# Kernel tuning notes

Hardware: AMD Instinct MI355X
Metric: run time of the kernel (lower is better)

The kernel has to match this reference:

```python
import jax, jax.numpy as jnp
import numpy as np

B, S, D = 4, 2048, 1024
H = 16
HD = D // H  # 64
FF = 4096


def setup_inputs() -> dict:
    key = jax.random.key(0)
    ks = jax.random.split(key, 11)
    sd = 1.0 / np.sqrt(D)
    inp = {
        "embeddings": jax.random.normal(ks[0], (B, S, D), dtype=jnp.float32),
        # per-head Linear weights stacked: [H, head_dim, D] (torch Linear layout)
        "Wq": jax.random.uniform(ks[1], (H, HD, D), jnp.float32, -sd, sd),
        "bq": jax.random.uniform(ks[2], (H, HD), jnp.float32, -sd, sd),
        "Wk": jax.random.uniform(ks[3], (H, HD, D), jnp.float32, -sd, sd),
        "bk": jax.random.uniform(ks[4], (H, HD), jnp.float32, -sd, sd),
        "Wv": jax.random.uniform(ks[5], (H, HD, D), jnp.float32, -sd, sd),
        "bv": jax.random.uniform(ks[6], (H, HD), jnp.float32, -sd, sd),
        "W1": jax.random.uniform(ks[7], (FF, D), jnp.float32, -sd, sd),
        "b1": jax.random.uniform(ks[8], (FF,), jnp.float32, -sd, sd),
        "W2": jax.random.uniform(ks[9], (D, FF), jnp.float32, -1.0 / np.sqrt(FF), 1.0 / np.sqrt(FF)),
        "b2": jax.random.uniform(ks[10], (D,), jnp.float32, -1.0 / np.sqrt(FF), 1.0 / np.sqrt(FF)),
    }
    return inp


def reference(embeddings, Wq, bq, Wk, bk, Wv, bv, W1, b1, W2, b2):
    # Per-head projections, batched over heads: [B,H,S,HD]
    Q = jnp.einsum("bsd,hed->bhse", embeddings, Wq) + bq[None, :, None, :]
    K = jnp.einsum("bsd,hed->bhse", embeddings, Wk) + bk[None, :, None, :]
    V = jnp.einsum("bsd,hed->bhse", embeddings, Wv) + bv[None, :, None, :]
    # NOTE: original scales by sqrt(embed_dim), not sqrt(head_dim)
    scale = 1.0 / jnp.sqrt(jnp.asarray(D, embeddings.dtype))
    scores = jnp.einsum("bhse,bhte->bhst", Q, K) * scale  # [B,H,S,S]
    A = jax.nn.softmax(scores, axis=-1)
    Hh = jnp.einsum("bhst,bhte->bhse", A, V)  # [B,H,S,HD]
    # concat heads along last dim (head order matches torch.cat)
    Hcat = jnp.transpose(Hh, (0, 2, 1, 3)).reshape(B, S, D)
    hid = jax.nn.relu(Hcat @ W1.T + b1)
    return hid @ W2.T + b2
```

## Files before the change

### kernel.cpp

```cpp
#include <hip/hip_runtime.h>
#include <stdint.h>


typedef __attribute__((ext_vector_type(8))) short bf16x8;
typedef __attribute__((ext_vector_type(4))) float f32x4;

__device__ __forceinline__ float bf2f(unsigned short u) {
  union { float f; uint32_t i; } v; v.i = ((uint32_t)u) << 16; return v.f;
}
__device__ __forceinline__ unsigned short f2bf(float f) {
  union { float f; uint32_t i; } v; v.f = f;
  uint32_t i = v.i;
  return (unsigned short)((i + 0x7fffu + ((i >> 16) & 1u)) >> 16);
}

#if __has_builtin(__builtin_amdgcn_exp2f)
#define EXP2(x) __builtin_amdgcn_exp2f(x)
#else
#define EXP2(x) __expf((x) * 0.6931471805599453f)
#endif

__device__ __forceinline__ uint32_t pk_bf16(float p0, float p1) {
  union { float f; uint32_t i; } a, b; a.f = p0; b.f = p1;
  return __builtin_amdgcn_perm(b.i + 0x8000u, a.i + 0x8000u, 0x07060302u);
}

__device__ __forceinline__ void gld16(const void* g, void* l) {
  __builtin_amdgcn_global_load_lds(
      (const __attribute__((address_space(1))) uint32_t*)(uintptr_t)g,
      (__attribute__((address_space(3))) uint32_t*)(uintptr_t)l, 16, 0, 0);
}

#define SCALE_Q 0.04508422002778011f

#define W1B          0
#define W2B    4194304
#define B1B    8388608
#define B2B    8392704
#define BQB    8393728
#define BKB    8394752
#define BVB    8395776
#define EMBB   8396800
#define WQB   16785408
#define WKB   17833984
#define WVB   18882560
#define QOFF  19931136
#define KOFF  28319744
#define VTOFF 36708352
#define HCOFF 45096960
#define HIDOFF 8396800

__global__ void cvt_all(const float* __restrict__ emb, const float* __restrict__ Wq,
                        const float* __restrict__ bq,  const float* __restrict__ Wk,
                        const float* __restrict__ bk,  const float* __restrict__ Wv,
                        const float* __restrict__ bv,  const float* __restrict__ W1,
                        const float* __restrict__ b1,  const float* __restrict__ W2,
                        const float* __restrict__ b2,  unsigned short* __restrict__ ws) {
  const int i4 = blockIdx.x * 256 + threadIdx.x;
  if (i4 >= 4982784) return;
  const float* s; unsigned short* d; int base;
  if      (i4 < 2097152) { s = emb; d = ws + EMBB; base = 0; }
  else if (i4 < 2359296) { s = Wq;  d = ws + WQB;  base = 2097152; }
  else if (i4 < 2621440) { s = Wk;  d = ws + WKB;  base = 2359296; }
  else if (i4 < 2883584) { s = Wv;  d = ws + WVB;  base = 2621440; }
  else if (i4 < 3932160) { s = W1;  d = ws + W1B;  base = 2883584; }
  else if (i4 < 4980736) { s = W2;  d = ws + W2B;  base = 3932160; }
  else if (i4 < 4980992) { s = bq;  d = ws + BQB;  base = 4980736; }
  else if (i4 < 4981248) { s = bk;  d = ws + BKB;  base = 4980992; }
  else if (i4 < 4981504) { s = bv;  d = ws + BVB;  base = 4981248; }
  else if (i4 < 4982528) { s = b1;  d = ws + B1B;  base = 4981504; }
  else                   { s = b2;  d = ws + B2B;  base = 4982528; }
  const int j = i4 - base;
  const float4 v = ((const float4*)s)[j];
  ushort4 o;
  o.x = f2bf(v.x); o.y = f2bf(v.y); o.z = f2bf(v.z); o.w = f2bf(v.w);
  *(ushort4*)(d + (size_t)j * 4) = o;
}

template <int MODE>
__launch_bounds__(256, 4)
__global__ void gemm128(const unsigned short* __restrict__ A,
                        const unsigned short* __restrict__ W0,
                        const unsigned short* __restrict__ W1p,
                        const unsigned short* __restrict__ W2p,
                        const unsigned short* __restrict__ bias0,
                        const unsigned short* __restrict__ bias1,
                        const unsigned short* __restrict__ bias2,
                        unsigned short* __restrict__ out0,
                        unsigned short* __restrict__ out1,
                        unsigned short* __restrict__ out2,
                        float* __restrict__ foutp,
                        int N, int K) {
  __shared__ unsigned short At[128 * 64];
  __shared__ unsigned short Bt[128 * 64];
  const int tid  = threadIdx.x;
  const int wave = tid >> 6, lane = tid & 63;
  const int quad = lane >> 4, l15 = lane & 15;

  const int lid = blockIdx.x + blockIdx.y * gridDim.x;
  const int s_ = lid >> 3;
  const int rowBase = (((lid & 7) + ((s_ & 7) << 3)) << 7);
  const int colBase = ((s_ >> 3) << 7);

  const unsigned short* W = W0;
  const unsigned short* bias = bias0;
  int colW = colBase;
  if (MODE == 2) {
    const int which = colBase >> 10;
    if (which == 1) { W = W1p; bias = bias1; }
    if (which == 2) { W = W2p; bias = bias2; }
    colW = colBase & 1023;
  }

  const unsigned short* gA[4]; const unsigned short* gB[4];
  unsigned short *lA[4], *lB[4];
#pragma unroll
  for (int i = 0; i < 4; ++i) {
    const int u = tid + 256 * i;
    const int r = u >> 3, e = (((u & 7) ^ (r & 7)) * 8);
    gA[i] = A + (size_t)(rowBase + r) * K + e;
    gB[i] = W + (size_t)(colW + r) * K + e;
    lA[i] = At + u * 8;
    lB[i] = Bt + u * 8;
  }

  const int wrow = (wave & 1) * 64, wcol = (wave >> 1) * 64;
  int aoff[2][4], boff[2][4];
#pragma unroll
  for (int kk = 0; kk < 2; ++kk)
#pragma unroll
    for (int t = 0; t < 4; ++t) {
      const int ra = wrow + t * 16 + l15;
      aoff[kk][t] = ra * 64 + (((quad + 4 * kk) ^ (ra & 7)) * 8);
      const int rb = wcol + t * 16 + l15;
      boff[kk][t] = rb * 64 + (((quad + 4 * kk) ^ (rb & 7)) * 8);
    }

  f32x4 acc[4][4] = {};
  for (int k0 = 0; k0 < K; k0 += 64) {
    __syncthreads();
#pragma unroll
    for (int i = 0; i < 4; ++i) { gld16(gA[i], lA[i]); gld16(gB[i], lB[i]); }
#pragma unroll
    for (int i = 0; i < 4; ++i) { gA[i] += 64; gB[i] += 64; }
    __syncthreads();
#pragma unroll
    for (int kk = 0; kk < 2; ++kk) {
      bf16x8 af[4], bfr[4];
#pragma unroll
      for (int t = 0; t < 4; ++t) af[t]  = *(const bf16x8*)(At + aoff[kk][t]);
#pragma unroll
      for (int t = 0; t < 4; ++t) bfr[t] = *(const bf16x8*)(Bt + boff[kk][t]);
#pragma unroll
      for (int mt = 0; mt < 4; ++mt)
#pragma unroll
        for (int nt = 0; nt < 4; ++nt)
          acc[mt][nt] = __builtin_amdgcn_mfma_f32_16x16x32_bf16(
              af[mt], bfr[nt], acc[mt][nt], 0, 0, 0);
    }
  }

#pragma unroll
  for (int mt = 0; mt < 4; ++mt) {
    const int row = rowBase + wrow + mt * 16 + quad * 4;
#pragma unroll
    for (int nt = 0; nt < 4; ++nt) {
      const int cIn = colW + wcol + nt * 16 + l15;
      const float bv = bf2f(bias[cIn]);
      if (MODE == 2) {
        const int which = colBase >> 10;
        const int h = cIn >> 6, e = cIn & 63;
#pragma unroll
        for (int r = 0; r < 4; ++r) {
          const int tok = row + r;
          const int b = tok >> 11, s = tok & 2047;
          const float v = acc[mt][nt][r] + bv;
          const size_t bh = (size_t)(b * 16 + h);
          if (which == 0)      out0[(bh * 2048 + s) * 64 + e] = f2bf(v * SCALE_Q);
          else if (which == 1) out1[(bh * 2048 + s) * 64 + e] = f2bf(v);
          else                 out2[(bh * 64 + e) * 2048 + s] = f2bf(v);
        }
      } else if (MODE == 1) {
#pragma unroll
        for (int r = 0; r < 4; ++r) {
          const float v = fmaxf(acc[mt][nt][r] + bv, 0.0f);
          out0[(size_t)(row + r) * N + cIn] = f2bf(v);
        }
      } else {
#pragma unroll
        for (int r = 0; r < 4; ++r)
          foutp[(size_t)(row + r) * N + cIn] = acc[mt][nt][r] + bv;
      }
    }
  }
}

__launch_bounds__(256, 4)
__global__ void flash_attn(const unsigned short* __restrict__ Q,
                           const unsigned short* __restrict__ Kg,
                           const unsigned short* __restrict__ Vt,
                           unsigned short* __restrict__ Hc) {
  __shared__ unsigned short Kt[64 * 64];
  __shared__ unsigned short Vs[64 * 64];
  __shared__ unsigned short Pl[4][32 * 64];
  __shared__ float Lb[4][32];
  const int tid  = threadIdx.x;
  const int wave = tid >> 6, lane = tid & 63;
  const int quad = lane >> 4, l15 = lane & 15;

  const int lid = blockIdx.x + blockIdx.y * gridDim.x;
  const int s_ = lid >> 3;
  const int bh = (lid & 7) + ((s_ & 7) << 3);
  const int q0 = ((s_ >> 3) << 7) + wave * 32;

  const size_t base = (size_t)bh * (2048 * 64);
  const unsigned short* Qb = Q  + base;
  const unsigned short* Kb = Kg + base;
  const unsigned short* Vb = Vt + base;

  bf16x8 qf[2][2];
#pragma unroll
  for (int qt = 0; qt < 2; ++qt) {
    const int q = q0 + qt * 16 + l15;
#pragma unroll
    for (int kk = 0; kk < 2; ++kk)
      qf[qt][kk] = *(const bf16x8*)(Qb + (size_t)q * 64 + kk * 32 + quad * 8);
  }

  const int u0 = tid, u1 = tid + 256;
  const int kr0 = u0 >> 3, kc0 = (((u0 & 7) ^ (kr0 & 7)) * 8);
  const int kr1 = u1 >> 3, kc1 = (((u1 & 7) ^ (kr1 & 7)) * 8);
  const unsigned short* gK0 = Kb + (size_t)kr0 * 64 + kc0;
  const unsigned short* gK1 = Kb + (size_t)kr1 * 64 + kc1;
  const unsigned short* gV0 = Vb + (size_t)kr0 * 2048 + kc0;
  const unsigned short* gV1 = Vb + (size_t)kr1 * 2048 + kc1;
  unsigned short* lK0 = Kt + u0 * 8;
  unsigned short* lK1 = Kt + u1 * 8;
  unsigned short* lV0 = Vs + u0 * 8;
  unsigned short* lV1 = Vs + u1 * 8;

  float l_acc[2] = {0.0f, 0.0f};
  f32x4 o[2][4] = {};
  unsigned short* Pw = Pl[wave];

  for (int it = 0; it < 32; ++it) {
    __syncthreads();
    gld16(gK0, lK0); gld16(gK1, lK1);
    gld16(gV0, lV0); gld16(gV1, lV1);
    gK0 += 4096; gK1 += 4096; gV0 += 64; gV1 += 64;
    __syncthreads();

    f32x4 st[4][2] = {};
#pragma unroll
    for (int tt = 0; tt < 4; ++tt) {
      const int t = tt * 16 + l15;
      const bf16x8 kf0 = *(const bf16x8*)(Kt + t * 64 + ((quad       ^ (t & 7)) * 8));
      const bf16x8 kf1 = *(const bf16x8*)(Kt + t * 64 + (((quad + 4) ^ (t & 7)) * 8));
#pragma unroll
      for (int qt = 0; qt < 2; ++qt) {
        st[tt][qt] = __builtin_amdgcn_mfma_f32_16x16x32_bf16(kf0, qf[qt][0], st[tt][qt], 0, 0, 0);
        st[tt][qt] = __builtin_amdgcn_mfma_f32_16x16x32_bf16(kf1, qf[qt][1], st[tt][qt], 0, 0, 0);
      }
    }

#pragma unroll
    for (int tt = 0; tt < 4; ++tt) {
      const int tc = tt * 2 + (quad >> 1);
#pragma unroll
      for (int qt = 0; qt < 2; ++qt) {
        const float p0 = EXP2(st[tt][qt][0]);
        const float p1 = EXP2(st[tt][qt][1]);
        const float p2 = EXP2(st[tt][qt][2]);
        const float p3 = EXP2(st[tt][qt][3]);
        l_acc[qt] += (p0 + p1) + (p2 + p3);
        uint2 w;
        w.x = pk_bf16(p0, p1);
        w.y = pk_bf16(p2, p3);
        const int qrow = qt * 16 + l15;
        *(uint2*)(Pw + qrow * 64 + ((tc ^ (qrow & 7)) * 8) + (quad & 1) * 4) = w;
      }
    }

    bf16x8 pf[2][2];
#pragma unroll
    for (int mt = 0; mt < 2; ++mt) {
      const int qq = mt * 16 + l15;
      pf[mt][0] = *(const bf16x8*)(Pw + qq * 64 + ((quad       ^ (qq & 7)) * 8));
      pf[mt][1] = *(const bf16x8*)(Pw + qq * 64 + (((quad + 4) ^ (qq & 7)) * 8));
    }
#pragma unroll
    for (int nt = 0; nt < 4; ++nt) {
      const int e = nt * 16 + l15;
      const bf16x8 vf0 = *(const bf16x8*)(Vs + e * 64 + ((quad       ^ (e & 7)) * 8));
      const bf16x8 vf1 = *(const bf16x8*)(Vs + e * 64 + (((quad + 4) ^ (e & 7)) * 8));
#pragma unroll
      for (int mt = 0; mt < 2; ++mt) {
        o[mt][nt] = __builtin_amdgcn_mfma_f32_16x16x32_bf16(pf[mt][0], vf0, o[mt][nt], 0, 0, 0);
        o[mt][nt] = __builtin_amdgcn_mfma_f32_16x16x32_bf16(pf[mt][1], vf1, o[mt][nt], 0, 0, 0);
      }
    }
  }

#pragma unroll
  for (int qt = 0; qt < 2; ++qt) {
    float v = l_acc[qt];
    v += __shfl_xor(v, 16, 64);
    v += __shfl_xor(v, 32, 64);
    Lb[wave][qt * 16 + l15] = v;
  }
  const f32x4 lv0 = *(const f32x4*)&Lb[wave][quad * 4];
  const f32x4 lv1 = *(const f32x4*)&Lb[wave][16 + quad * 4];

  const int b = bh >> 4, h = bh & 15;
#pragma unroll
  for (int mt = 0; mt < 2; ++mt)
#pragma unroll
    for (int r = 0; r < 4; ++r) {
      const int qg = q0 + mt * 16 + quad * 4 + r;
      const float inv = __builtin_amdgcn_rcpf(mt == 0 ? lv0[r] : lv1[r]);
#pragma unroll
      for (int nt = 0; nt < 4; ++nt) {
        const int e = nt * 16 + l15;
        Hc[((size_t)b * 2048 + qg) * 1024 + h * 64 + e] = f2bf(o[mt][nt][r] * inv);
      }
    }
}

extern "C" void kernel_launch(void* const* d_in, const int* in_sizes, int n_in,
                              void* d_out, int out_size, void* d_ws, size_t ws_size,
                              hipStream_t stream) {
  const float* emb = (const float*)d_in[0];
  const float* Wq  = (const float*)d_in[1];
  const float* bq  = (const float*)d_in[2];
  const float* Wk  = (const float*)d_in[3];
  const float* bk  = (const float*)d_in[4];
  const float* Wv  = (const float*)d_in[5];
  const float* bv  = (const float*)d_in[6];
  const float* W1  = (const float*)d_in[7];
  const float* b1  = (const float*)d_in[8];
  const float* W2  = (const float*)d_in[9];
  const float* b2  = (const float*)d_in[10];

  unsigned short* ws = (unsigned short*)d_ws;
  float* out = (float*)d_out;

  cvt_all<<<19465, 256, 0, stream>>>(emb, Wq, bq, Wk, bk, Wv, bv, W1, b1, W2, b2, ws);
  gemm128<2><<<dim3(24, 64), 256, 0, stream>>>(
      ws + EMBB, ws + WQB, ws + WKB, ws + WVB, ws + BQB, ws + BKB, ws + BVB,
      ws + QOFF, ws + KOFF, ws + VTOFF, nullptr, 3072, 1024);
  flash_attn<<<dim3(16, 64), 256, 0, stream>>>(ws + QOFF, ws + KOFF, ws + VTOFF, ws + HCOFF);
  gemm128<1><<<dim3(32, 64), 256, 0, stream>>>(
      ws + HCOFF, ws + W1B, nullptr, nullptr, ws + B1B, nullptr, nullptr,
      ws + HIDOFF, nullptr, nullptr, nullptr, 4096, 1024);
  gemm128<0><<<dim3(8, 64), 256, 0, stream>>>(
      ws + HIDOFF, ws + W2B, nullptr, nullptr, ws + B2B, nullptr, nullptr,
      nullptr, nullptr, nullptr, out, 1024, 4096);
}
```

Baseline: 405.6 us.

## Double-buffer K tiles, overlap V loads, compute row sums via MFMA

The attention kernel now double-buffers K in shared memory, prefetching the next K tile during the current QK^T compute. V is loaded after the PV step, and explicit vmcnt waits with raw barriers replace the two full syncthreads per iteration. The softmax row sum is now computed by an MFMA against a vector of ones, which removes the scalar accumulation and the shuffle/LDS reduction. It also uses the hardware bf16 pack instruction and raises wave priority around MFMA blocks. The trade-offs are more shared memory and hand-written wait counts that must match the issued loads exactly, plus a row sum taken from bf16-rounded probabilities.

```diff
diff --git a/kernel.cpp b/kernel.cpp
--- a/kernel.cpp
+++ b/kernel.cpp
@@ -20,9 +20,10 @@
 #define EXP2(x) __expf((x) * 0.6931471805599453f)
 #endif
 
-__device__ __forceinline__ uint32_t pk_bf16(float p0, float p1) {
-  union { float f; uint32_t i; } a, b; a.f = p0; b.f = p1;
-  return __builtin_amdgcn_perm(b.i + 0x8000u, a.i + 0x8000u, 0x07060302u);
+__device__ __forceinline__ uint32_t cvtpk(float p0, float p1) {
+  uint32_t r;
+  asm("v_cvt_pk_bf16_f32 %0, %1, %2" : "=v"(r) : "v"(p0), "v"(p1));
+  return r;
 }
 
 __device__ __forceinline__ void gld16(const void* g, void* l) {
@@ -200,10 +201,9 @@
                            const unsigned short* __restrict__ Kg,
                            const unsigned short* __restrict__ Vt,
                            unsigned short* __restrict__ Hc) {
-  __shared__ unsigned short Kt[64 * 64];
+  __shared__ unsigned short Kt[2 * 64 * 64];
   __shared__ unsigned short Vs[64 * 64];
   __shared__ unsigned short Pl[4][32 * 64];
-  __shared__ float Lb[4][32];
   const int tid  = threadIdx.x;
   const int wave = tid >> 6, lane = tid & 63;
   const int quad = lane >> 4, l15 = lane & 15;
@@ -239,29 +239,38 @@
   unsigned short* lV0 = Vs + u0 * 8;
   unsigned short* lV1 = Vs + u1 * 8;
 
-  float l_acc[2] = {0.0f, 0.0f};
+  gld16(gK0, lK0); gld16(gK1, lK1);
+  gld16(gV0, lV0); gld16(gV1, lV1);
+  gK0 += 4096; gK1 += 4096; gV0 += 64; gV1 += 64;
+  __syncthreads();
+
+  const short oneb = (short)0x3F80;
+  const bf16x8 ones = {oneb, oneb, oneb, oneb, oneb, oneb, oneb, oneb};
   f32x4 o[2][4] = {};
+  f32x4 lacc[2] = {};
   unsigned short* Pw = Pl[wave];
 
   for (int it = 0; it < 32; ++it) {
-    __syncthreads();
-    gld16(gK0, lK0); gld16(gK1, lK1);
-    gld16(gV0, lV0); gld16(gV1, lV1);
-    gK0 += 4096; gK1 += 4096; gV0 += 64; gV1 += 64;
-    __syncthreads();
+    const int nb = ((it + 1) & 1) * 4096;
+    gld16(gK0, lK0 + nb); gld16(gK1, lK1 + nb);
+    gK0 += 4096; gK1 += 4096;
+
+    const unsigned short* Kc = Kt + (it & 1) * 4096;
 
     f32x4 st[4][2] = {};
+    __builtin_amdgcn_s_setprio(1);
 #pragma unroll
     for (int tt = 0; tt < 4; ++tt) {
       const int t = tt * 16 + l15;
-      const bf16x8 kf0 = *(const bf16x8*)(Kt + t * 64 + ((quad       ^ (t & 7)) * 8));
-      const bf16x8 kf1 = *(const bf16x8*)(Kt + t * 64 + (((quad + 4) ^ (t & 7)) * 8));
+      const bf16x8 kf0 = *(const bf16x8*)(Kc + t * 64 + ((quad       ^ (t & 7)) * 8));
+      const bf16x8 kf1 = *(const bf16x8*)(Kc + t * 64 + (((quad + 4) ^ (t & 7)) * 8));
 #pragma unroll
       for (int qt = 0; qt < 2; ++qt) {
         st[tt][qt] = __builtin_amdgcn_mfma_f32_16x16x32_bf16(kf0, qf[qt][0], st[tt][qt], 0, 0, 0);
         st[tt][qt] = __builtin_amdgcn_mfma_f32_16x16x32_bf16(kf1, qf[qt][1], st[tt][qt], 0, 0, 0);
       }
     }
+    __builtin_amdgcn_s_setprio(0);
 
 #pragma unroll
     for (int tt = 0; tt < 4; ++tt) {
@@ -272,14 +281,16 @@
         const float p1 = EXP2(st[tt][qt][1]);
         const float p2 = EXP2(st[tt][qt][2]);
         const float p3 = EXP2(st[tt][qt][3]);
-        l_acc[qt] += (p0 + p1) + (p2 + p3);
         uint2 w;
-        w.x = pk_bf16(p0, p1);
-        w.y = pk_bf16(p2, p3);
+        w.x = cvtpk(p0, p1);
+        w.y = cvtpk(p2, p3);
         const int qrow = qt * 16 + l15;
         *(uint2*)(Pw + qrow * 64 + ((tc ^ (qrow & 7)) * 8) + (quad & 1) * 4) = w;
       }
     }
+
+    asm volatile("s_waitcnt vmcnt(2)" ::: "memory");
+    __builtin_amdgcn_s_barrier();
 
     bf16x8 pf[2][2];
 #pragma unroll
@@ -288,6 +299,7 @@
       pf[mt][0] = *(const bf16x8*)(Pw + qq * 64 + ((quad       ^ (qq & 7)) * 8));
       pf[mt][1] = *(const bf16x8*)(Pw + qq * 64 + (((quad + 4) ^ (qq & 7)) * 8));
     }
+    __builtin_amdgcn_s_setprio(1);
 #pragma unroll
     for (int nt = 0; nt < 4; ++nt) {
       const int e = nt * 16 + l15;
@@ -299,17 +311,21 @@
         o[mt][nt] = __builtin_amdgcn_mfma_f32_16x16x32_bf16(pf[mt][1], vf1, o[mt][nt], 0, 0, 0);
       }
     }
-  }
-
-#pragma unroll
-  for (int qt = 0; qt < 2; ++qt) {
-    float v = l_acc[qt];
-    v += __shfl_xor(v, 16, 64);
-    v += __shfl_xor(v, 32, 64);
-    Lb[wave][qt * 16 + l15] = v;
-  }
-  const f32x4 lv0 = *(const f32x4*)&Lb[wave][quad * 4];
-  const f32x4 lv1 = *(const f32x4*)&Lb[wave][16 + quad * 4];
+#pragma unroll
+    for (int mt = 0; mt < 2; ++mt) {
+      lacc[mt] = __builtin_amdgcn_mfma_f32_16x16x32_bf16(pf[mt][0], ones, lacc[mt], 0, 0, 0);
+      lacc[mt] = __builtin_amdgcn_mfma_f32_16x16x32_bf16(pf[mt][1], ones, lacc[mt], 0, 0, 0);
+    }
+    __builtin_amdgcn_s_setprio(0);
+
+    asm volatile("s_waitcnt vmcnt(0)" ::: "memory");
+    __builtin_amdgcn_s_barrier();
+
+    if (it < 31) {
+      gld16(gV0, lV0); gld16(gV1, lV1);
+      gV0 += 64; gV1 += 64;
+    }
+  }
 
   const int b = bh >> 4, h = bh & 15;
 #pragma unroll
@@ -317,7 +333,7 @@
 #pragma unroll
     for (int r = 0; r < 4; ++r) {
       const int qg = q0 + mt * 16 + quad * 4 + r;
-      const float inv = __builtin_amdgcn_rcpf(mt == 0 ? lv0[r] : lv1[r]);
+      const float inv = __builtin_amdgcn_rcpf(lacc[mt][r]);
 #pragma unroll
       for (int nt = 0; nt < 4; ++nt) {
         const int e = nt * 16 + l15;
```

Result: no change. 404.4 us (median of 3 runs) (-0.3%).
